# Kernel optimization log

Hardware: AMD Instinct MI355X
Metric: run time of the kernel (lower is better)

Reference implementation:

```python
import jax, jax.numpy as jnp
import numpy as np

B, N, D_IN, L, H, NB = 4, 512, 32, 64, 128, 2

def setup_inputs() -> dict:
    key = jax.random.key(0)
    ks = jax.random.split(key, 8)
    s = lambda k, shape, fan: jax.random.normal(k, shape, dtype=jnp.float32) / np.float32(np.sqrt(fan))
    return {
        "X": jax.random.normal(ks[0], (B, N, D_IN), dtype=jnp.float32),
        "proj_w": s(ks[1], (D_IN, L), D_IN),
        "proj_b": jnp.zeros((L,), jnp.float32),
        "rn_w1": s(ks[2], (NB, 2 * L, H), 2 * L),
        "rn_b1": jnp.zeros((NB, H), jnp.float32),
        "rn_w2": s(ks[3], (NB, H, L), H),
        "rn_b2": jnp.zeros((NB, L), jnp.float32),
        "fc_w1": s(ks[4], (NB, L, H), L),
        "fc_b1": jnp.zeros((NB, H), jnp.float32),
        "fc_w2": s(ks[5], (NB, H, L), H),
        "fc_b2": jnp.zeros((NB, L), jnp.float32),
        "dec_w": s(ks[6], (L, 1), L),
        "dec_b": jnp.zeros((1,), jnp.float32),
    }

def _rn_block(Z, rw1, rb1, rw2, rb2, fw1, fb1, fw2, fb2):
    # RelationNetwork: pairs[b,n,m] = concat(Y[b,m], X[b,n]) with X=Y=Z.
    # First linear on concat splits into two small GEMMs (Y-half of rw1 first).
    Ldim = Z.shape[-1]
    M = Z.shape[1]
    y_lin = Z @ rw1[:Ldim]          # [B,M,H]  (Y occupies first L cols of pairs)
    x_lin = Z @ rw1[Ldim:]          # [B,N,H]
    h = jax.nn.relu(x_lin[:, :, None, :] + y_lin[:, None, :, :] + rb1)  # [B,N,M,H]
    # sum-pool over M commutes with the second linear layer
    rn_out = h.sum(axis=2) @ rw2 + M * rb2  # [B,N,L]
    Z = Z + rn_out
    Z = Z + (jax.nn.relu(Z @ fw1 + fb1) @ fw2 + fb2)
    return Z

def reference(X, proj_w, proj_b, rn_w1, rn_b1, rn_w2, rn_b2, fc_w1, fc_b1, fc_w2, fc_b2, dec_w, dec_b):
    Z = X @ proj_w + proj_b  # [B,N,L]
    for i in range(rn_w1.shape[0]):  # fixed small num_blocks
        Z = _rn_block(Z, rn_w1[i], rn_b1[i], rn_w2[i], rn_b2[i],
                      fc_w1[i], fc_b1[i], fc_w2[i], fc_b2[i])
    pooled = Z.sum(axis=1)           # pool2='sum' over set dim
    out = pooled @ dec_w + dec_b     # [B,1]
    return out.squeeze(-1)           # [B]
```

## Files before the change

kernel.cpp:

```cpp
#include <hip/hip_runtime.h>
#include <math.h>

#define B 4
#define N 512
#define DIN 32
#define L 64
#define H 128
#define NB 2
#define R (B * N)

__global__ void k_proj_lin(const float* __restrict__ X, const float* __restrict__ PW,
                           const float* __restrict__ PB, const float* __restrict__ w1,
                           const float* __restrict__ b1, float* __restrict__ Z,
                           float* __restrict__ ylin, float* __restrict__ xlin,
                           float* __restrict__ out) {
    int r = threadIdx.x / 128;
    int t = threadIdx.x % 128;
    int row = blockIdx.x * 2 + r;
    __shared__ float zrow[2][L];

    if (blockIdx.x == 0 && threadIdx.x < B) out[threadIdx.x] = 0.f;

    if (t < L) {
        const float* x = X + row * DIN;
        float acc = PB[t];
#pragma unroll
        for (int k = 0; k < DIN; ++k) acc += x[k] * PW[k * L + t];
        zrow[r][t] = acc;
        Z[row * L + t] = acc;
    }
    __syncthreads();
    float ay = b1[t];
    float ax = 0.f;
#pragma unroll
    for (int k = 0; k < L; ++k) {
        float zv = zrow[r][k];
        ay += zv * w1[k * H + t];
        ax += zv * w1[(L + k) * H + t];
    }
    ylin[row * H + t] = ay;
    xlin[row * H + t] = ax;
}

__global__ void k_pairsort(const float* __restrict__ xlin, const float* __restrict__ ylin,
                           float* __restrict__ hsum) {
    __shared__ float ys[1024];
    __shared__ float ss[N + 1];
    __shared__ float csum[64];
    __shared__ float csuf[65];

    int t = threadIdx.x;
    int b = blockIdx.x >> 7;
    int h = blockIdx.x & 127;

    const float* ycol = ylin + (size_t)b * N * H + h;
    for (int m = t; m < N; m += 256) ys[m] = ycol[(size_t)m * H];
    for (int m = N + t; m < 1024; m += 256) ys[m] = INFINITY;
    __syncthreads();

    for (int k = 2; k <= N; k <<= 1) {
        for (int j = k >> 1; j > 0; j >>= 1) {
            int i = ((t & ~(j - 1)) << 1) | (t & (j - 1));
            int p = i | j;
            float a = ys[i], c = ys[p];
            bool up = (i & k) == 0;
            if ((a > c) == up) { ys[i] = c; ys[p] = a; }
            __syncthreads();
        }
    }

    if (t < 64) {
        float s = 0.f;
        int base = t * 8;
#pragma unroll
        for (int q = 7; q >= 0; --q) s += ys[base + q];
        csum[t] = s;
    }
    __syncthreads();
    if (t == 0) {
        csuf[64] = 0.f;
        float run = 0.f;
        for (int c = 63; c >= 0; --c) { run += csum[c]; csuf[c] = run; }
    }
    __syncthreads();
    for (int i = t; i < N; i += 256) {
        float s = csuf[(i >> 3) + 1];
        int e = i | 7;
        for (int q = e; q >= i; --q) s += ys[q];
        ss[i] = s;
    }
    if (t == 0) ss[N] = 0.f;
    __syncthreads();

    const float* xcol = xlin + (size_t)b * N * H + h;
    float* ocol = hsum + (size_t)b * N * H + h;
    int n0 = t, n1 = t + 256;
    float x0 = xcol[(size_t)n0 * H];
    float x1 = xcol[(size_t)n1 * H];
    float v0 = -x0, v1 = -x1;
    int p0 = 0, p1 = 0;
#pragma unroll
    for (int s = 512; s >= 1; s >>= 1) {
        if (ys[p0 + s - 1] <= v0) p0 += s;
        if (ys[p1 + s - 1] <= v1) p1 += s;
    }
    ocol[(size_t)n0 * H] = (float)(N - p0) * x0 + ss[p0];
    ocol[(size_t)n1 * H] = (float)(N - p1) * x1 + ss[p1];
}

template <bool FINAL>
__global__ void k_post(const float* __restrict__ hsum, const float* __restrict__ w2,
                       const float* __restrict__ b2, const float* __restrict__ fw1,
                       const float* __restrict__ fb1, const float* __restrict__ fw2,
                       const float* __restrict__ fb2, const float* __restrict__ nw1,
                       const float* __restrict__ nb1, float* __restrict__ Z,
                       float* __restrict__ ylin, float* __restrict__ xlin,
                       const float* __restrict__ dw, const float* __restrict__ db,
                       float* __restrict__ out) {
    __shared__ float wbuf[H * L];
    __shared__ float hl_[8][H];
    __shared__ float zl[8][L];
    __shared__ float tl[8][H];
    __shared__ float part[4];

    int t = threadIdx.x;
    int row0 = blockIdx.x * 8;

    ((float4*)hl_)[t] = ((const float4*)(hsum + (size_t)row0 * H))[t];
    if (t < 128) ((float4*)zl)[t] = ((const float4*)(Z + (size_t)row0 * L))[t];
#pragma unroll
    for (int j = 0; j < 8; ++j)
        ((float4*)wbuf)[t + j * 256] = ((const float4*)w2)[t + j * 256];
    __syncthreads();

    {
        int l = t & 63;
        int r0 = (t >> 6) * 2, r1 = r0 + 1;
        float a0 = 0.f, a1 = 0.f;
#pragma unroll
        for (int kk = 0; kk < H; kk += 4) {
            float4 h0v = *(float4*)&hl_[r0][kk];
            float4 h1v = *(float4*)&hl_[r1][kk];
            float w0 = wbuf[(kk + 0) * L + l];
            float w1v = wbuf[(kk + 1) * L + l];
            float w2v = wbuf[(kk + 2) * L + l];
            float w3 = wbuf[(kk + 3) * L + l];
            a0 += h0v.x * w0 + h0v.y * w1v + h0v.z * w2v + h0v.w * w3;
            a1 += h1v.x * w0 + h1v.y * w1v + h1v.z * w2v + h1v.w * w3;
        }
        float nb2 = (float)N * b2[l];
        zl[r0][l] += a0 + nb2;
        zl[r1][l] += a1 + nb2;
    }
    __syncthreads();
#pragma unroll
    for (int j = 0; j < 8; ++j)
        ((float4*)wbuf)[t + j * 256] = ((const float4*)fw1)[t + j * 256];
    __syncthreads();

    {
        int h = t & 127;
        int rq = (t >> 7) * 4;
        float acc0 = 0.f, acc1 = 0.f, acc2 = 0.f, acc3 = 0.f;
#pragma unroll
        for (int ll = 0; ll < L; ll += 4) {
            float w0 = wbuf[(ll + 0) * H + h];
            float w1v = wbuf[(ll + 1) * H + h];
            float w2v = wbuf[(ll + 2) * H + h];
            float w3 = wbuf[(ll + 3) * H + h];
            float4 z0 = *(float4*)&zl[rq + 0][ll];
            float4 z1 = *(float4*)&zl[rq + 1][ll];
            float4 z2 = *(float4*)&zl[rq + 2][ll];
            float4 z3 = *(float4*)&zl[rq + 3][ll];
            acc0 += z0.x * w0 + z0.y * w1v + z0.z * w2v + z0.w * w3;
            acc1 += z1.x * w0 + z1.y * w1v + z1.z * w2v + z1.w * w3;
            acc2 += z2.x * w0 + z2.y * w1v + z2.z * w2v + z2.w * w3;
            acc3 += z3.x * w0 + z3.y * w1v + z3.z * w2v + z3.w * w3;
        }
        float bb = fb1[h];
        tl[rq + 0][h] = fmaxf(acc0 + bb, 0.f);
        tl[rq + 1][h] = fmaxf(acc1 + bb, 0.f);
        tl[rq + 2][h] = fmaxf(acc2 + bb, 0.f);
        tl[rq + 3][h] = fmaxf(acc3 + bb, 0.f);
    }
    __syncthreads();
#pragma unroll
    for (int j = 0; j < 8; ++j)
        ((float4*)wbuf)[t + j * 256] = ((const float4*)fw2)[t + j * 256];
    __syncthreads();

    float zfin0, zfin1;
    int l_ = t & 63;
    int r0_ = (t >> 6) * 2, r1_ = r0_ + 1;
    {
        float a0 = 0.f, a1 = 0.f;
#pragma unroll
        for (int kk = 0; kk < H; kk += 4) {
            float4 t0v = *(float4*)&tl[r0_][kk];
            float4 t1v = *(float4*)&tl[r1_][kk];
            float w0 = wbuf[(kk + 0) * L + l_];
            float w1v = wbuf[(kk + 1) * L + l_];
            float w2v = wbuf[(kk + 2) * L + l_];
            float w3 = wbuf[(kk + 3) * L + l_];
            a0 += t0v.x * w0 + t0v.y * w1v + t0v.z * w2v + t0v.w * w3;
            a1 += t1v.x * w0 + t1v.y * w1v + t1v.z * w2v + t1v.w * w3;
        }
        float bb = fb2[l_];
        zfin0 = zl[r0_][l_] + a0 + bb;
        zfin1 = zl[r1_][l_] + a1 + bb;
    }

    if (FINAL) {
        float v = (zfin0 + zfin1) * dw[l_];
#pragma unroll
        for (int off = 32; off > 0; off >>= 1) v += __shfl_down(v, off);
        if (l_ == 0) part[t >> 6] = v;
        __syncthreads();
        if (t == 0) {
            float s = part[0] + part[1] + part[2] + part[3];
            if ((row0 % N) == 0) s += db[0];
            atomicAdd(out + row0 / N, s);
        }
        return;
    }

    __syncthreads();
    zl[r0_][l_] = zfin0;
    zl[r1_][l_] = zfin1;
    Z[(size_t)(row0 + r0_) * L + l_] = zfin0;
    Z[(size_t)(row0 + r1_) * L + l_] = zfin1;
    __syncthreads();

#pragma unroll
    for (int j = 0; j < 8; ++j)
        ((float4*)wbuf)[t + j * 256] = ((const float4*)nw1)[t + j * 256];
    __syncthreads();
    {
        int h = t & 127;
        int rq = (t >> 7) * 4;
        float acc0 = nb1[h], acc1 = acc0, acc2 = acc0, acc3 = acc0;
#pragma unroll
        for (int kk = 0; kk < L; kk += 4) {
            float w0 = wbuf[(kk + 0) * H + h];
            float w1v = wbuf[(kk + 1) * H + h];
            float w2v = wbuf[(kk + 2) * H + h];
            float w3 = wbuf[(kk + 3) * H + h];
            float4 z0 = *(float4*)&zl[rq + 0][kk];
            float4 z1 = *(float4*)&zl[rq + 1][kk];
            float4 z2 = *(float4*)&zl[rq + 2][kk];
            float4 z3 = *(float4*)&zl[rq + 3][kk];
            acc0 += z0.x * w0 + z0.y * w1v + z0.z * w2v + z0.w * w3;
            acc1 += z1.x * w0 + z1.y * w1v + z1.z * w2v + z1.w * w3;
            acc2 += z2.x * w0 + z2.y * w1v + z2.z * w2v + z2.w * w3;
            acc3 += z3.x * w0 + z3.y * w1v + z3.z * w2v + z3.w * w3;
        }
        ylin[(size_t)(row0 + rq + 0) * H + h] = acc0;
        ylin[(size_t)(row0 + rq + 1) * H + h] = acc1;
        ylin[(size_t)(row0 + rq + 2) * H + h] = acc2;
        ylin[(size_t)(row0 + rq + 3) * H + h] = acc3;
    }
    __syncthreads();
#pragma unroll
    for (int j = 0; j < 8; ++j)
        ((float4*)wbuf)[t + j * 256] = ((const float4*)(nw1 + L * H))[t + j * 256];
    __syncthreads();
    {
        int h = t & 127;
        int rq = (t >> 7) * 4;
        float acc0 = 0.f, acc1 = 0.f, acc2 = 0.f, acc3 = 0.f;
#pragma unroll
        for (int kk = 0; kk < L; kk += 4) {
            float w0 = wbuf[(kk + 0) * H + h];
            float w1v = wbuf[(kk + 1) * H + h];
            float w2v = wbuf[(kk + 2) * H + h];
            float w3 = wbuf[(kk + 3) * H + h];
            float4 z0 = *(float4*)&zl[rq + 0][kk];
            float4 z1 = *(float4*)&zl[rq + 1][kk];
            float4 z2 = *(float4*)&zl[rq + 2][kk];
            float4 z3 = *(float4*)&zl[rq + 3][kk];
            acc0 += z0.x * w0 + z0.y * w1v + z0.z * w2v + z0.w * w3;
            acc1 += z1.x * w0 + z1.y * w1v + z1.z * w2v + z1.w * w3;
            acc2 += z2.x * w0 + z2.y * w1v + z2.z * w2v + z2.w * w3;
            acc3 += z3.x * w0 + z3.y * w1v + z3.z * w2v + z3.w * w3;
        }
        xlin[(size_t)(row0 + rq + 0) * H + h] = acc0;
        xlin[(size_t)(row0 + rq + 1) * H + h] = acc1;
        xlin[(size_t)(row0 + rq + 2) * H + h] = acc2;
        xlin[(size_t)(row0 + rq + 3) * H + h] = acc3;
    }
}

extern "C" void kernel_launch(void* const* d_in, const int* in_sizes, int n_in,
                              void* d_out, int out_size, void* d_ws, size_t ws_size,
                              hipStream_t stream) {
    const float* X      = (const float*)d_in[0];
    const float* proj_w = (const float*)d_in[1];
    const float* proj_b = (const float*)d_in[2];
    const float* rn_w1  = (const float*)d_in[3];
    const float* rn_b1  = (const float*)d_in[4];
    const float* rn_w2  = (const float*)d_in[5];
    const float* rn_b2  = (const float*)d_in[6];
    const float* fc_w1  = (const float*)d_in[7];
    const float* fc_b1  = (const float*)d_in[8];
    const float* fc_w2  = (const float*)d_in[9];
    const float* fc_b2  = (const float*)d_in[10];
    const float* dec_w  = (const float*)d_in[11];
    const float* dec_b  = (const float*)d_in[12];
    float* out = (float*)d_out;

    float* ws   = (float*)d_ws;
    float* Z    = ws;
    float* ylin = Z + R * L;
    float* xlin = ylin + R * H;
    float* hsum = xlin + R * H;

    k_proj_lin<<<R / 2, 256, 0, stream>>>(X, proj_w, proj_b, rn_w1, rn_b1, Z, ylin, xlin, out);
    k_pairsort<<<B * H, 256, 0, stream>>>(xlin, ylin, hsum);
    k_post<false><<<R / 8, 256, 0, stream>>>(hsum, rn_w2, rn_b2, fc_w1, fc_b1, fc_w2, fc_b2,
                                             rn_w1 + 2 * L * H, rn_b1 + H, Z, ylin, xlin,
                                             nullptr, nullptr, nullptr);
    k_pairsort<<<B * H, 256, 0, stream>>>(xlin, ylin, hsum);
    k_post<true><<<R / 8, 256, 0, stream>>>(hsum, rn_w2 + H * L, rn_b2 + L,
                                            fc_w1 + L * H, fc_b1 + H, fc_w2 + H * L, fc_b2 + L,
                                            nullptr, nullptr, Z, nullptr, nullptr,
                                            dec_w, dec_b, out);
}
```

Before: 60.11 us.

## Fold input projection into first pair-sort kernel and drop separate projection launch

The projection kernel is removed. The first pair kernel now precomposes proj_w with the two halves of rn_w1 per column h, producing 32+2 coefficient vectors, and computes ylin/xlin for its column straight from X. The first post kernel recomputes Z from X and proj_w in shared memory instead of reading it from global memory. This cuts one launch and the global round trip for Z, ylin and xlin in block 0, at the cost of redundant per-block projection work and a slightly different float summation order.

```diff
diff --git a/kernel.cpp b/kernel.cpp
--- a/kernel.cpp
+++ b/kernel.cpp
@@ -9,52 +9,59 @@
 #define NB 2
 #define R (B * N)
 
-__global__ void k_proj_lin(const float* __restrict__ X, const float* __restrict__ PW,
-                           const float* __restrict__ PB, const float* __restrict__ w1,
-                           const float* __restrict__ b1, float* __restrict__ Z,
-                           float* __restrict__ ylin, float* __restrict__ xlin,
-                           float* __restrict__ out) {
-    int r = threadIdx.x / 128;
-    int t = threadIdx.x % 128;
-    int row = blockIdx.x * 2 + r;
-    __shared__ float zrow[2][L];
-
-    if (blockIdx.x == 0 && threadIdx.x < B) out[threadIdx.x] = 0.f;
-
-    if (t < L) {
-        const float* x = X + row * DIN;
-        float acc = PB[t];
-#pragma unroll
-        for (int k = 0; k < DIN; ++k) acc += x[k] * PW[k * L + t];
-        zrow[r][t] = acc;
-        Z[row * L + t] = acc;
-    }
-    __syncthreads();
-    float ay = b1[t];
-    float ax = 0.f;
-#pragma unroll
-    for (int k = 0; k < L; ++k) {
-        float zv = zrow[r][k];
-        ay += zv * w1[k * H + t];
-        ax += zv * w1[(L + k) * H + t];
-    }
-    ylin[row * H + t] = ay;
-    xlin[row * H + t] = ax;
-}
-
-__global__ void k_pairsort(const float* __restrict__ xlin, const float* __restrict__ ylin,
-                           float* __restrict__ hsum) {
+__global__ void k_pair0(const float* __restrict__ X, const float* __restrict__ PW,
+                        const float* __restrict__ PB, const float* __restrict__ w1,
+                        const float* __restrict__ rb1, float* __restrict__ hsum,
+                        float* __restrict__ out) {
     __shared__ float ys[1024];
     __shared__ float ss[N + 1];
     __shared__ float csum[64];
     __shared__ float csuf[65];
+    __shared__ float vu[66];
 
     int t = threadIdx.x;
     int b = blockIdx.x >> 7;
     int h = blockIdx.x & 127;
 
-    const float* ycol = ylin + (size_t)b * N * H + h;
-    for (int m = t; m < N; m += 256) ys[m] = ycol[(size_t)m * H];
+    if (blockIdx.x == 0 && t < B) out[t] = 0.f;
+
+    if (t < 64) {
+        int d = t & 31;
+        const float* wcol = w1 + (t < 32 ? 0 : L * H) + h;
+        float s = 0.f;
+#pragma unroll
+        for (int k = 0; k < L; ++k) s += PW[d * L + k] * wcol[(size_t)k * H];
+        vu[t] = s;
+    } else if (t < 66) {
+        const float* wcol = w1 + (t == 64 ? 0 : L * H) + h;
+        float s = (t == 64) ? rb1[h] : 0.f;
+#pragma unroll
+        for (int k = 0; k < L; ++k) s += PB[k] * wcol[(size_t)k * H];
+        vu[t] = s;
+    }
+    __syncthreads();
+
+    float xq0, xq1;
+    {
+        const float* xr = X + ((size_t)b * N + t) * DIN;
+        float ya = vu[64], xa = vu[65];
+#pragma unroll
+        for (int d = 0; d < DIN; ++d) {
+            float xv = xr[d];
+            ya += xv * vu[d];
+            xa += xv * vu[32 + d];
+        }
+        ys[t] = ya; xq0 = xa;
+        const float* xr2 = X + ((size_t)b * N + t + 256) * DIN;
+        float yb = vu[64], xb = vu[65];
+#pragma unroll
+        for (int d = 0; d < DIN; ++d) {
+            float xv = xr2[d];
+            yb += xv * vu[d];
+            xb += xv * vu[32 + d];
+        }
+        ys[t + 256] = yb; xq1 = xb;
+    }
     for (int m = N + t; m < 1024; m += 256) ys[m] = INFINITY;
     __syncthreads();
 
@@ -92,6 +99,68 @@
     if (t == 0) ss[N] = 0.f;
     __syncthreads();
 
+    float* ocol = hsum + (size_t)b * N * H + h;
+    float v0 = -xq0, v1 = -xq1;
+    int p0 = 0, p1 = 0;
+#pragma unroll
+    for (int s = 512; s >= 1; s >>= 1) {
+        if (ys[p0 + s - 1] <= v0) p0 += s;
+        if (ys[p1 + s - 1] <= v1) p1 += s;
+    }
+    ocol[(size_t)t * H] = (float)(N - p0) * xq0 + ss[p0];
+    ocol[(size_t)(t + 256) * H] = (float)(N - p1) * xq1 + ss[p1];
+}
+
+__global__ void k_pair1(const float* __restrict__ xlin, const float* __restrict__ ylin,
+                        float* __restrict__ hsum) {
+    __shared__ float ys[1024];
+    __shared__ float ss[N + 1];
+    __shared__ float csum[64];
+    __shared__ float csuf[65];
+
+    int t = threadIdx.x;
+    int b = blockIdx.x >> 7;
+    int h = blockIdx.x & 127;
+
+    const float* ycol = ylin + (size_t)b * N * H + h;
+    for (int m = t; m < N; m += 256) ys[m] = ycol[(size_t)m * H];
+    for (int m = N + t; m < 1024; m += 256) ys[m] = INFINITY;
+    __syncthreads();
+
+    for (int k = 2; k <= N; k <<= 1) {
+        for (int j = k >> 1; j > 0; j >>= 1) {
+            int i = ((t & ~(j - 1)) << 1) | (t & (j - 1));
+            int p = i | j;
+            float a = ys[i], c = ys[p];
+            bool up = (i & k) == 0;
+            if ((a > c) == up) { ys[i] = c; ys[p] = a; }
+            __syncthreads();
+        }
+    }
+
+    if (t < 64) {
+        float s = 0.f;
+        int base = t * 8;
+#pragma unroll
+        for (int q = 7; q >= 0; --q) s += ys[base + q];
+        csum[t] = s;
+    }
+    __syncthreads();
+    if (t == 0) {
+        csuf[64] = 0.f;
+        float run = 0.f;
+        for (int c = 63; c >= 0; --c) { run += csum[c]; csuf[c] = run; }
+    }
+    __syncthreads();
+    for (int i = t; i < N; i += 256) {
+        float s = csuf[(i >> 3) + 1];
+        int e = i | 7;
+        for (int q = e; q >= i; --q) s += ys[q];
+        ss[i] = s;
+    }
+    if (t == 0) ss[N] = 0.f;
+    __syncthreads();
+
     const float* xcol = xlin + (size_t)b * N * H + h;
     float* ocol = hsum + (size_t)b * N * H + h;
     int n0 = t, n1 = t + 256;
@@ -108,26 +177,49 @@
     ocol[(size_t)n1 * H] = (float)(N - p1) * x1 + ss[p1];
 }
 
-template <bool FINAL>
+template <bool FINAL, bool FROMX>
 __global__ void k_post(const float* __restrict__ hsum, const float* __restrict__ w2,
                        const float* __restrict__ b2, const float* __restrict__ fw1,
                        const float* __restrict__ fb1, const float* __restrict__ fw2,
                        const float* __restrict__ fb2, const float* __restrict__ nw1,
                        const float* __restrict__ nb1, float* __restrict__ Z,
                        float* __restrict__ ylin, float* __restrict__ xlin,
+                       const float* __restrict__ X, const float* __restrict__ PW,
+                       const float* __restrict__ PB,
                        const float* __restrict__ dw, const float* __restrict__ db,
                        float* __restrict__ out) {
     __shared__ float wbuf[H * L];
-    __shared__ float hl_[8][H];
-    __shared__ float zl[8][L];
-    __shared__ float tl[8][H];
+    __shared__ float hl_[8 * H];
+    __shared__ float zl[8 * L];
+    __shared__ float tl[8 * H];
     __shared__ float part[4];
 
     int t = threadIdx.x;
     int row0 = blockIdx.x * 8;
 
     ((float4*)hl_)[t] = ((const float4*)(hsum + (size_t)row0 * H))[t];
-    if (t < 128) ((float4*)zl)[t] = ((const float4*)(Z + (size_t)row0 * L))[t];
+    if (FROMX) {
+        ((float4*)wbuf)[t] = ((const float4*)PW)[t];
+        ((float4*)wbuf)[t + 256] = ((const float4*)PW)[t + 256];
+        if (t < 64) ((float4*)tl)[t] = ((const float4*)(X + (size_t)row0 * DIN))[t];
+        __syncthreads();
+        {
+            int l = t & 63;
+            int r0 = (t >> 6) * 2, r1 = r0 + 1;
+            float a0 = PB[l], a1 = a0;
+#pragma unroll
+            for (int d = 0; d < DIN; ++d) {
+                float w = wbuf[d * L + l];
+                a0 += tl[r0 * DIN + d] * w;
+                a1 += tl[r1 * DIN + d] * w;
+            }
+            zl[r0 * L + l] = a0;
+            zl[r1 * L + l] = a1;
+        }
+        __syncthreads();
+    } else {
+        if (t < 128) ((float4*)zl)[t] = ((const float4*)(Z + (size_t)row0 * L))[t];
+    }
 #pragma unroll
     for (int j = 0; j < 8; ++j)
         ((float4*)wbuf)[t + j * 256] = ((const float4*)w2)[t + j * 256];
@@ -139,8 +231,8 @@
         float a0 = 0.f, a1 = 0.f;
 #pragma unroll
         for (int kk = 0; kk < H; kk += 4) {
-            float4 h0v = *(float4*)&hl_[r0][kk];
-            float4 h1v = *(float4*)&hl_[r1][kk];
+            float4 h0v = *(float4*)&hl_[r0 * H + kk];
+            float4 h1v = *(float4*)&hl_[r1 * H + kk];
             float w0 = wbuf[(kk + 0) * L + l];
             float w1v = wbuf[(kk + 1) * L + l];
             float w2v = wbuf[(kk + 2) * L + l];
@@ -149,8 +241,8 @@
             a1 += h1v.x * w0 + h1v.y * w1v + h1v.z * w2v + h1v.w * w3;
         }
         float nb2 = (float)N * b2[l];
-        zl[r0][l] += a0 + nb2;
-        zl[r1][l] += a1 + nb2;
+        zl[r0 * L + l] += a0 + nb2;
+        zl[r1 * L + l] += a1 + nb2;
     }
     __syncthreads();
 #pragma unroll
@@ -168,20 +260,20 @@
             float w1v = wbuf[(ll + 1) * H + h];
             float w2v = wbuf[(ll + 2) * H + h];
             float w3 = wbuf[(ll + 3) * H + h];
-            float4 z0 = *(float4*)&zl[rq + 0][ll];
-            float4 z1 = *(float4*)&zl[rq + 1][ll];
-            float4 z2 = *(float4*)&zl[rq + 2][ll];
-            float4 z3 = *(float4*)&zl[rq + 3][ll];
+            float4 z0 = *(float4*)&zl[(rq + 0) * L + ll];
+            float4 z1 = *(float4*)&zl[(rq + 1) * L + ll];
+            float4 z2 = *(float4*)&zl[(rq + 2) * L + ll];
+            float4 z3 = *(float4*)&zl[(rq + 3) * L + ll];
             acc0 += z0.x * w0 + z0.y * w1v + z0.z * w2v + z0.w * w3;
             acc1 += z1.x * w0 + z1.y * w1v + z1.z * w2v + z1.w * w3;
             acc2 += z2.x * w0 + z2.y * w1v + z2.z * w2v + z2.w * w3;
             acc3 += z3.x * w0 + z3.y * w1v + z3.z * w2v + z3.w * w3;
         }
         float bb = fb1[h];
-        tl[rq + 0][h] = fmaxf(acc0 + bb, 0.f);
-        tl[rq + 1][h] = fmaxf(acc1 + bb, 0.f);
-        tl[rq + 2][h] = fmaxf(acc2 + bb, 0.f);
-        tl[rq + 3][h] = fmaxf(acc3 + bb, 0.f);
+        tl[(rq + 0) * H + h] = fmaxf(acc0 + bb, 0.f);
+        tl[(rq + 1) * H + h] = fmaxf(acc1 + bb, 0.f);
+        tl[(rq + 2) * H + h] = fmaxf(acc2 + bb, 0.f);
+        tl[(rq + 3) * H + h] = fmaxf(acc3 + bb, 0.f);
     }
     __syncthreads();
 #pragma unroll
@@ -196,8 +288,8 @@
         float a0 = 0.f, a1 = 0.f;
 #pragma unroll
         for (int kk = 0; kk < H; kk += 4) {
-            float4 t0v = *(float4*)&tl[r0_][kk];
-            float4 t1v = *(float4*)&tl[r1_][kk];
+            float4 t0v = *(float4*)&tl[r0_ * H + kk];
+            float4 t1v = *(float4*)&tl[r1_ * H + kk];
             float w0 = wbuf[(kk + 0) * L + l_];
             float w1v = wbuf[(kk + 1) * L + l_];
             float w2v = wbuf[(kk + 2) * L + l_];
@@ -206,8 +298,8 @@
             a1 += t1v.x * w0 + t1v.y * w1v + t1v.z * w2v + t1v.w * w3;
         }
         float bb = fb2[l_];
-        zfin0 = zl[r0_][l_] + a0 + bb;
-        zfin1 = zl[r1_][l_] + a1 + bb;
+        zfin0 = zl[r0_ * L + l_] + a0 + bb;
+        zfin1 = zl[r1_ * L + l_] + a1 + bb;
     }
 
     if (FINAL) {
@@ -225,8 +317,8 @@
     }
 
     __syncthreads();
-    zl[r0_][l_] = zfin0;
-    zl[r1_][l_] = zfin1;
+    zl[r0_ * L + l_] = zfin0;
+    zl[r1_ * L + l_] = zfin1;
     Z[(size_t)(row0 + r0_) * L + l_] = zfin0;
     Z[(size_t)(row0 + r1_) * L + l_] = zfin1;
     __syncthreads();
@@ -245,10 +337,10 @@
             float w1v = wbuf[(kk + 1) * H + h];
             float w2v = wbuf[(kk + 2) * H + h];
             float w3 = wbuf[(kk + 3) * H + h];
-            float4 z0 = *(float4*)&zl[rq + 0][kk];
-            float4 z1 = *(float4*)&zl[rq + 1][kk];
-            float4 z2 = *(float4*)&zl[rq + 2][kk];
-            float4 z3 = *(float4*)&zl[rq + 3][kk];
+            float4 z0 = *(float4*)&zl[(rq + 0) * L + kk];
+            float4 z1 = *(float4*)&zl[(rq + 1) * L + kk];
+            float4 z2 = *(float4*)&zl[(rq + 2) * L + kk];
+            float4 z3 = *(float4*)&zl[(rq + 3) * L + kk];
             acc0 += z0.x * w0 + z0.y * w1v + z0.z * w2v + z0.w * w3;
             acc1 += z1.x * w0 + z1.y * w1v + z1.z * w2v + z1.w * w3;
             acc2 += z2.x * w0 + z2.y * w1v + z2.z * w2v + z2.w * w3;
@@ -274,10 +366,10 @@
             float w1v = wbuf[(kk + 1) * H + h];
             float w2v = wbuf[(kk + 2) * H + h];
             float w3 = wbuf[(kk + 3) * H + h];
-            float4 z0 = *(float4*)&zl[rq + 0][kk];
-            float4 z1 = *(float4*)&zl[rq + 1][kk];
-            float4 z2 = *(float4*)&zl[rq + 2][kk];
-            float4 z3 = *(float4*)&zl[rq + 3][kk];
+            float4 z0 = *(float4*)&zl[(rq + 0) * L + kk];
+            float4 z1 = *(float4*)&zl[(rq + 1) * L + kk];
+            float4 z2 = *(float4*)&zl[(rq + 2) * L + kk];
+            float4 z3 = *(float4*)&zl[(rq + 3) * L + kk];
             acc0 += z0.x * w0 + z0.y * w1v + z0.z * w2v + z0.w * w3;
             acc1 += z1.x * w0 + z1.y * w1v + z1.z * w2v + z1.w * w3;
             acc2 += z2.x * w0 + z2.y * w1v + z2.z * w2v + z2.w * w3;
@@ -314,14 +406,14 @@
     float* xlin = ylin + R * H;
     float* hsum = xlin + R * H;
 
-    k_proj_lin<<<R / 2, 256, 0, stream>>>(X, proj_w, proj_b, rn_w1, rn_b1, Z, ylin, xlin, out);
-    k_pairsort<<<B * H, 256, 0, stream>>>(xlin, ylin, hsum);
-    k_post<false><<<R / 8, 256, 0, stream>>>(hsum, rn_w2, rn_b2, fc_w1, fc_b1, fc_w2, fc_b2,
-                                             rn_w1 + 2 * L * H, rn_b1 + H, Z, ylin, xlin,
-                                             nullptr, nullptr, nullptr);
-    k_pairsort<<<B * H, 256, 0, stream>>>(xlin, ylin, hsum);
-    k_post<true><<<R / 8, 256, 0, stream>>>(hsum, rn_w2 + H * L, rn_b2 + L,
-                                            fc_w1 + L * H, fc_b1 + H, fc_w2 + H * L, fc_b2 + L,
-                                            nullptr, nullptr, Z, nullptr, nullptr,
-                                            dec_w, dec_b, out);
+    k_pair0<<<B * H, 256, 0, stream>>>(X, proj_w, proj_b, rn_w1, rn_b1, hsum, out);
+    k_post<false, true><<<R / 8, 256, 0, stream>>>(
+        hsum, rn_w2, rn_b2, fc_w1, fc_b1, fc_w2, fc_b2,
+        rn_w1 + 2 * L * H, rn_b1 + H, Z, ylin, xlin,
+        X, proj_w, proj_b, nullptr, nullptr, nullptr);
+    k_pair1<<<B * H, 256, 0, stream>>>(xlin, ylin, hsum);
+    k_post<true, false><<<R / 8, 256, 0, stream>>>(
+        hsum, rn_w2 + H * L, rn_b2 + L, fc_w1 + L * H, fc_b1 + H,
+        fc_w2 + H * L, fc_b2 + L, nullptr, nullptr, Z, nullptr, nullptr,
+        nullptr, nullptr, nullptr, dec_w, dec_b, out);
 }
```

New measurement: 61.82 us. +2.8%, slower.

## Sort ylin in 64-element chunks and binary-search each chunk

Applied to the files above, without the earlier changes.

Replaces the full 512-element bitonic sort per (batch, hidden) column with eight independent 64-element bitonic sorts. Each chunk gets its own suffix sums, built in parallel instead of by a serial loop on one thread. Each query now binary-searches all eight chunks and adds up the counts and suffix sums. This removes many barrier-separated sort stages and the serial prefix scan. In exchange, each query does more search steps and shared-memory lookups.

```diff
diff --git a/kernel.cpp b/kernel.cpp
--- a/kernel.cpp
+++ b/kernel.cpp
@@ -44,26 +44,26 @@
 
 __global__ void k_pairsort(const float* __restrict__ xlin, const float* __restrict__ ylin,
                            float* __restrict__ hsum) {
-    __shared__ float ys[1024];
-    __shared__ float ss[N + 1];
+    __shared__ float ys[512];
+    __shared__ float ss[8 * 65];
     __shared__ float csum[64];
-    __shared__ float csuf[65];
+    __shared__ float csuf[8 * 9];
 
     int t = threadIdx.x;
     int b = blockIdx.x >> 7;
     int h = blockIdx.x & 127;
 
     const float* ycol = ylin + (size_t)b * N * H + h;
-    for (int m = t; m < N; m += 256) ys[m] = ycol[(size_t)m * H];
-    for (int m = N + t; m < 1024; m += 256) ys[m] = INFINITY;
-    __syncthreads();
-
-    for (int k = 2; k <= N; k <<= 1) {
+    ys[t] = ycol[(size_t)t * H];
+    ys[t + 256] = ycol[(size_t)(t + 256) * H];
+    __syncthreads();
+
+    for (int k = 2; k <= 64; k <<= 1) {
         for (int j = k >> 1; j > 0; j >>= 1) {
             int i = ((t & ~(j - 1)) << 1) | (t & (j - 1));
             int p = i | j;
             float a = ys[i], c = ys[p];
-            bool up = (i & k) == 0;
+            bool up = (i & k & 63) == 0;
             if ((a > c) == up) { ys[i] = c; ys[p] = a; }
             __syncthreads();
         }
@@ -77,35 +77,46 @@
         csum[t] = s;
     }
     __syncthreads();
-    if (t == 0) {
-        csuf[64] = 0.f;
-        float run = 0.f;
-        for (int c = 63; c >= 0; --c) { run += csum[c]; csuf[c] = run; }
-    }
-    __syncthreads();
-    for (int i = t; i < N; i += 256) {
-        float s = csuf[(i >> 3) + 1];
-        int e = i | 7;
-        for (int q = e; q >= i; --q) s += ys[q];
-        ss[i] = s;
-    }
-    if (t == 0) ss[N] = 0.f;
+    if (t < 64) {
+        int c = t >> 3, s = t & 7;
+        float acc = 0.f;
+        for (int q = 7; q >= s; --q) acc += csum[c * 8 + q];
+        csuf[c * 9 + s] = acc;
+    }
+    if (t < 8) csuf[t * 9 + 8] = 0.f;
+    __syncthreads();
+    for (int i = t; i < 512; i += 256) {
+        int c = i >> 6, loc = i & 63;
+        float s = csuf[c * 9 + (loc >> 3) + 1];
+        int base = c * 64;
+        int e = loc | 7;
+        for (int q = e; q >= loc; --q) s += ys[base + q];
+        ss[c * 65 + loc] = s;
+    }
+    if (t < 8) ss[t * 65 + 64] = 0.f;
     __syncthreads();
 
     const float* xcol = xlin + (size_t)b * N * H + h;
     float* ocol = hsum + (size_t)b * N * H + h;
-    int n0 = t, n1 = t + 256;
-    float x0 = xcol[(size_t)n0 * H];
-    float x1 = xcol[(size_t)n1 * H];
+    float x0 = xcol[(size_t)t * H];
+    float x1 = xcol[(size_t)(t + 256) * H];
     float v0 = -x0, v1 = -x1;
-    int p0 = 0, p1 = 0;
-#pragma unroll
-    for (int s = 512; s >= 1; s >>= 1) {
-        if (ys[p0 + s - 1] <= v0) p0 += s;
-        if (ys[p1 + s - 1] <= v1) p1 += s;
-    }
-    ocol[(size_t)n0 * H] = (float)(N - p0) * x0 + ss[p0];
-    ocol[(size_t)n1 * H] = (float)(N - p1) * x1 + ss[p1];
+    float acc0 = 0.f, acc1 = 0.f;
+    int cnt0 = 0, cnt1 = 0;
+#pragma unroll
+    for (int c = 0; c < 8; ++c) {
+        int base = c * 64;
+        int p0 = 0, p1 = 0;
+#pragma unroll
+        for (int s = 32; s >= 1; s >>= 1) {
+            if (ys[base + p0 + s - 1] <= v0) p0 += s;
+            if (ys[base + p1 + s - 1] <= v1) p1 += s;
+        }
+        cnt0 += 64 - p0; acc0 += ss[c * 65 + p0];
+        cnt1 += 64 - p1; acc1 += ss[c * 65 + p1];
+    }
+    ocol[(size_t)t * H] = (float)cnt0 * x0 + acc0;
+    ocol[(size_t)(t + 256) * H] = (float)cnt1 * x1 + acc1;
 }
 
 template <bool FINAL>
```

Result: faster. 57.05 us (median of 2 runs) (-5.1%).
